# Kernel optimization log

Hardware: AMD Instinct MI355X
Metric: run time of the kernel (lower is better)

The kernel has to match this reference:

```python
import jax, jax.numpy as jnp
import numpy as np

TOP_K = 2
NORM_MIN = 1e-12
B, S, H = 2, 1024, 2048
E, I = 16, 1024
SHARED_I = 2048  # moe_intermediate_size * moe_num_shared_experts


def setup_inputs() -> dict:
    key = jax.random.key(0)
    ks = jax.random.split(key, 8)
    s = 0.02  # init scale
    return {
        "hidden_states": jax.random.normal(ks[0], (B, S, H), jnp.float32),
        "router_w": jax.random.normal(ks[1], (E, H), jnp.float32) * s,
        "w_gate": jax.random.normal(ks[2], (E, H, I), jnp.float32) * s,
        "w_up": jax.random.normal(ks[3], (E, H, I), jnp.float32) * s,
        "w_down": jax.random.normal(ks[4], (E, I, H), jnp.float32) * s,
        "ws_gate": jax.random.normal(ks[5], (H, SHARED_I), jnp.float32) * s,
        "ws_up": jax.random.normal(ks[6], (H, SHARED_I), jnp.float32) * s,
        "ws_down": jax.random.normal(ks[7], (SHARED_I, H), jnp.float32) * s,
    }


def reference(hidden_states, router_w, w_gate, w_up, w_down, ws_gate, ws_up, ws_down):
    b, s, h = hidden_states.shape
    x = hidden_states.reshape(-1, h)                      # [N, H]
    n = x.shape[0]

    # Router: float32 softmax -> top-k -> renormalize with clamp
    router_logits = x.astype(jnp.float32) @ router_w.T    # [N, E]
    probs = jax.nn.softmax(router_logits, axis=-1)
    rw, sel = jax.lax.top_k(probs, TOP_K)                 # [N, K]
    rw = rw / jnp.clip(rw.sum(axis=-1, keepdims=True), NORM_MIN)
    rw = rw.astype(x.dtype)

    # Dense combine weights [N, E] (equivalent to one_hot dispatch/scatter)
    combine = jnp.zeros((n, E), x.dtype).at[jnp.arange(n)[:, None], sel].set(rw)

    # All-expert SwiGLU MLP (full-capacity MoE, no dropped tokens)
    g = jnp.einsum('nh,ehi->eni', x, w_gate)              # [E, N, I]
    u = jnp.einsum('nh,ehi->eni', x, w_up)
    o = jnp.einsum('eni,eih->enh', jax.nn.silu(g) * u, w_down)  # [E, N, H]
    out = jnp.einsum('enh,ne->nh', o, combine)            # weighted combine

    # Shared expert path
    shared = (jax.nn.silu(x @ ws_gate) * (x @ ws_up)) @ ws_down
    out = out + shared

    return out.reshape(b, s, h), router_logits
```

## Files before the change

kernel.cpp:

```cpp
#include <hip/hip_runtime.h>
#include <cstdint>
#include <cstddef>
#include <cmath>

#define N_TOK 2048
#define HDIM  2048
#define NEXP  16
#define IDIM  1024
#define SIDIM 2048
#define NTHREADS 256

typedef __attribute__((ext_vector_type(8))) short bf16x8;
typedef __attribute__((ext_vector_type(4))) float f32x4;

__device__ __forceinline__ uint32_t f2bf_u(float f) {
    union { float f; uint32_t u; } v; v.f = f;
    return (v.u + 0x7FFFu + ((v.u >> 16) & 1u)) >> 16;
}
__device__ __forceinline__ uint32_t pack2bf(float lo, float hi) {
    return f2bf_u(lo) | (f2bf_u(hi) << 16);
}

__global__ __launch_bounds__(NTHREADS)
void router_kernel(const float* __restrict__ x,
                   const float* __restrict__ rw,
                   float* __restrict__ logits_out,
                   int* __restrict__ cnt,
                   int* __restrict__ tok_list,
                   float* __restrict__ wt_list)
{
    const int n = blockIdx.x;
    const int tid = threadIdx.x;
    const float* xr = x + (size_t)n * HDIM;

    float acc[NEXP];
#pragma unroll
    for (int e = 0; e < NEXP; ++e) acc[e] = 0.f;

    for (int h = tid; h < HDIM; h += NTHREADS) {
        float xv = xr[h];
#pragma unroll
        for (int e = 0; e < NEXP; ++e) acc[e] += xv * rw[(size_t)e * HDIM + h];
    }

    __shared__ float red[NEXP][NTHREADS];
#pragma unroll
    for (int e = 0; e < NEXP; ++e) red[e][tid] = acc[e];
    __syncthreads();
    for (int s = NTHREADS / 2; s > 0; s >>= 1) {
        if (tid < s) {
#pragma unroll
            for (int e = 0; e < NEXP; ++e) red[e][tid] += red[e][tid + s];
        }
        __syncthreads();
    }

    if (tid < NEXP) logits_out[(size_t)n * NEXP + tid] = red[tid][0];

    if (tid == 0) {
        float l[NEXP];
#pragma unroll
        for (int e = 0; e < NEXP; ++e) l[e] = red[e][0];
        int e0 = 0;
#pragma unroll
        for (int e = 1; e < NEXP; ++e) if (l[e] > l[e0]) e0 = e;
        int e1 = (e0 == 0) ? 1 : 0;
#pragma unroll
        for (int e = 0; e < NEXP; ++e)
            if (e != e0 && l[e] > l[e1]) e1 = e;
        float t = expf(l[e1] - l[e0]);
        float s = 1.f + t;
        float rw0 = 1.f / s;
        float rw1 = t / s;
        int p0 = atomicAdd(&cnt[e0], 1);
        tok_list[e0 * N_TOK + p0] = n;
        wt_list[e0 * N_TOK + p0] = rw0;
        int p1 = atomicAdd(&cnt[e1], 1);
        tok_list[e1 * N_TOK + p1] = n;
        wt_list[e1 * N_TOK + p1] = rw1;
    }
}

__global__ void prefix_kernel(const int* __restrict__ cnt, int* __restrict__ base)
{
    if (threadIdx.x == 0) {
        int s = 0;
        for (int e = 0; e < NEXP; ++e) { base[e] = s; s += cnt[e]; }
    }
}

__global__ __launch_bounds__(NTHREADS)
void dual_swiglu_mfma(const float* __restrict__ X,
                      const float* __restrict__ WgAll,
                      const float* __restrict__ WuAll,
                      unsigned short* __restrict__ Y,
                      const int* __restrict__ cnt,
                      const int* __restrict__ base,
                      const int* __restrict__ tok_list,
                      const int Icols)
{
    const int e  = blockIdx.z;
    const int m0 = blockIdx.y * 128;
    const int n0 = blockIdx.x * 64;
    const bool gathered = (tok_list != nullptr);
    const int M = gathered ? cnt[e] : N_TOK;
    if (m0 >= M) return;
    const float* Wg = WgAll + (size_t)e * HDIM * Icols;
    const float* Wu = WuAll + (size_t)e * HDIM * Icols;
    const int yb = gathered ? base[e] : 0;

    __shared__ short As[128][40];
    __shared__ short Gs[64][40];
    __shared__ short Us[64][40];

    const int tid  = threadIdx.x;
    const int lane = tid & 63;
    const int wave = tid >> 6;
    const int wm   = wave >> 1;
    const int wn   = wave & 1;
    const int l15  = lane & 15;
    const int q    = lane >> 4;

    const int ar = tid >> 1;
    const int ac = (tid & 1) * 16;
    const int slotA = m0 + ar;
    int xrow;
    if (gathered) xrow = tok_list[e * N_TOK + ((slotA < M) ? slotA : 0)];
    else          xrow = slotA;
    const float* xp = X + (size_t)xrow * HDIM + ac;

    const int wng = (tid & 15) << 2;
    const int wkp = (tid >> 4) << 1;
    const float* gp = Wg + (size_t)wkp * Icols + n0 + wng;
    const float* up = Wu + (size_t)wkp * Icols + n0 + wng;

    f32x4 accg[4][2], accu[4][2];
#pragma unroll
    for (int i = 0; i < 4; ++i)
#pragma unroll
        for (int j = 0; j < 2; ++j) {
            accg[i][j] = (f32x4){0.f, 0.f, 0.f, 0.f};
            accu[i][j] = (f32x4){0.f, 0.f, 0.f, 0.f};
        }

    for (int k0 = 0; k0 < HDIM; k0 += 32) {
        const float* xk = xp + k0;
        float4 xa = *(const float4*)(xk + 0);
        float4 xb = *(const float4*)(xk + 4);
        float4 xc = *(const float4*)(xk + 8);
        float4 xd = *(const float4*)(xk + 12);
        const float* gk = gp + (size_t)k0 * Icols;
        float4 g0 = *(const float4*)(gk);
        float4 g1 = *(const float4*)(gk + Icols);
        const float* uk = up + (size_t)k0 * Icols;
        float4 u0 = *(const float4*)(uk);
        float4 u1 = *(const float4*)(uk + Icols);

        __syncthreads();
        {
            uint4 w0 = make_uint4(pack2bf(xa.x, xa.y), pack2bf(xa.z, xa.w),
                                  pack2bf(xb.x, xb.y), pack2bf(xb.z, xb.w));
            uint4 w1 = make_uint4(pack2bf(xc.x, xc.y), pack2bf(xc.z, xc.w),
                                  pack2bf(xd.x, xd.y), pack2bf(xd.z, xd.w));
            *reinterpret_cast<uint4*>(&As[ar][ac])     = w0;
            *reinterpret_cast<uint4*>(&As[ar][ac + 8]) = w1;
        }
        ((uint32_t*)&Gs[wng + 0][wkp])[0] = pack2bf(g0.x, g1.x);
        ((uint32_t*)&Gs[wng + 1][wkp])[0] = pack2bf(g0.y, g1.y);
        ((uint32_t*)&Gs[wng + 2][wkp])[0] = pack2bf(g0.z, g1.z);
        ((uint32_t*)&Gs[wng + 3][wkp])[0] = pack2bf(g0.w, g1.w);
        ((uint32_t*)&Us[wng + 0][wkp])[0] = pack2bf(u0.x, u1.x);
        ((uint32_t*)&Us[wng + 1][wkp])[0] = pack2bf(u0.y, u1.y);
        ((uint32_t*)&Us[wng + 2][wkp])[0] = pack2bf(u0.z, u1.z);
        ((uint32_t*)&Us[wng + 3][wkp])[0] = pack2bf(u0.w, u1.w);
        __syncthreads();

        bf16x8 af[4], bg[2], bu[2];
#pragma unroll
        for (int i = 0; i < 4; ++i)
            af[i] = *reinterpret_cast<const bf16x8*>(&As[wm * 64 + i * 16 + l15][q * 8]);
#pragma unroll
        for (int j = 0; j < 2; ++j) {
            bg[j] = *reinterpret_cast<const bf16x8*>(&Gs[wn * 32 + j * 16 + l15][q * 8]);
            bu[j] = *reinterpret_cast<const bf16x8*>(&Us[wn * 32 + j * 16 + l15][q * 8]);
        }
#pragma unroll
        for (int i = 0; i < 4; ++i)
#pragma unroll
            for (int j = 0; j < 2; ++j) {
                accg[i][j] = __builtin_amdgcn_mfma_f32_16x16x32_bf16(af[i], bg[j], accg[i][j], 0, 0, 0);
                accu[i][j] = __builtin_amdgcn_mfma_f32_16x16x32_bf16(af[i], bu[j], accu[i][j], 0, 0, 0);
            }
    }

#pragma unroll
    for (int i = 0; i < 4; ++i) {
#pragma unroll
        for (int r = 0; r < 4; ++r) {
            const int slot = m0 + wm * 64 + i * 16 + q * 4 + r;
            if (slot < M) {
                unsigned short* yrow = Y + (size_t)(yb + slot) * Icols;
#pragma unroll
                for (int j = 0; j < 2; ++j) {
                    const int col = n0 + wn * 32 + j * 16 + l15;
                    float g = accg[i][j][r];
                    float u = accu[i][j][r];
                    float y = (g / (1.f + expf(-g))) * u;
                    yrow[col] = (unsigned short)f2bf_u(y);
                }
            }
        }
    }
}

__global__ __launch_bounds__(NTHREADS)
void down_mfma(const unsigned short* __restrict__ A,
               const float* __restrict__ WdAll,
               float* __restrict__ out,
               const int* __restrict__ cnt,
               const int* __restrict__ base,
               const int* __restrict__ tok_list,
               const float* __restrict__ wt_list,
               const int K)
{
    const int e  = blockIdx.z;
    const int m0 = blockIdx.y * 128;
    const int n0 = blockIdx.x * 128;
    const bool scatter = (tok_list != nullptr);
    const int M = scatter ? cnt[e] : N_TOK;
    if (m0 >= M) return;
    const float* Wd = WdAll + (size_t)e * K * HDIM;
    const int yb = scatter ? base[e] : 0;

    __shared__ short As[128][40];
    __shared__ short Bs[128][40];

    const int tid  = threadIdx.x;
    const int lane = tid & 63;
    const int wave = tid >> 6;
    const int wm   = wave >> 1;
    const int wn   = wave & 1;
    const int l15  = lane & 15;
    const int q    = lane >> 4;

    const int ar = tid >> 1;
    const int ac = (tid & 1) * 16;
    const int slotA = m0 + ar;
    const int arow = yb + ((slotA < M) ? slotA : 0);
    const unsigned short* ap = A + (size_t)arow * K + ac;

    const int bn = (tid & 31) << 2;
    const int bk = (tid >> 5) << 2;
    const float* bp = Wd + (size_t)bk * HDIM + n0 + bn;

    f32x4 acc[4][4];
#pragma unroll
    for (int i = 0; i < 4; ++i)
#pragma unroll
        for (int j = 0; j < 4; ++j) acc[i][j] = (f32x4){0.f, 0.f, 0.f, 0.f};

    for (int k0 = 0; k0 < K; k0 += 32) {
        uint4 a0 = *(const uint4*)(ap + k0);
        uint4 a1 = *(const uint4*)(ap + k0 + 8);
        const float* bkp = bp + (size_t)k0 * HDIM;
        float4 b0 = *(const float4*)(bkp);
        float4 b1 = *(const float4*)(bkp + HDIM);
        float4 b2 = *(const float4*)(bkp + 2 * (size_t)HDIM);
        float4 b3 = *(const float4*)(bkp + 3 * (size_t)HDIM);

        __syncthreads();
        *reinterpret_cast<uint4*>(&As[ar][ac])     = a0;
        *reinterpret_cast<uint4*>(&As[ar][ac + 8]) = a1;
        {
            uint2 w;
            w.x = pack2bf(b0.x, b1.x); w.y = pack2bf(b2.x, b3.x);
            *reinterpret_cast<uint2*>(&Bs[bn + 0][bk]) = w;
            w.x = pack2bf(b0.y, b1.y); w.y = pack2bf(b2.y, b3.y);
            *reinterpret_cast<uint2*>(&Bs[bn + 1][bk]) = w;
            w.x = pack2bf(b0.z, b1.z); w.y = pack2bf(b2.z, b3.z);
            *reinterpret_cast<uint2*>(&Bs[bn + 2][bk]) = w;
            w.x = pack2bf(b0.w, b1.w); w.y = pack2bf(b2.w, b3.w);
            *reinterpret_cast<uint2*>(&Bs[bn + 3][bk]) = w;
        }
        __syncthreads();

        bf16x8 af[4], bf[4];
#pragma unroll
        for (int i = 0; i < 4; ++i)
            af[i] = *reinterpret_cast<const bf16x8*>(&As[wm * 64 + i * 16 + l15][q * 8]);
#pragma unroll
        for (int j = 0; j < 4; ++j)
            bf[j] = *reinterpret_cast<const bf16x8*>(&Bs[wn * 64 + j * 16 + l15][q * 8]);
#pragma unroll
        for (int i = 0; i < 4; ++i)
#pragma unroll
            for (int j = 0; j < 4; ++j)
                acc[i][j] = __builtin_amdgcn_mfma_f32_16x16x32_bf16(af[i], bf[j], acc[i][j], 0, 0, 0);
    }

#pragma unroll
    for (int i = 0; i < 4; ++i) {
#pragma unroll
        for (int r = 0; r < 4; ++r) {
            const int slot = m0 + wm * 64 + i * 16 + q * 4 + r;
            if (slot >= M) continue;
            if (scatter) {
                const int tok = tok_list[e * N_TOK + slot];
                const float wt = wt_list[e * N_TOK + slot];
                float* orow = out + (size_t)tok * HDIM;
#pragma unroll
                for (int j = 0; j < 4; ++j) {
                    const int col = n0 + wn * 64 + j * 16 + l15;
                    atomicAdd(&orow[col], wt * acc[i][j][r]);
                }
            } else {
                float* orow = out + (size_t)slot * HDIM;
#pragma unroll
                for (int j = 0; j < 4; ++j) {
                    const int col = n0 + wn * 64 + j * 16 + l15;
                    orow[col] = acc[i][j][r];
                }
            }
        }
    }
}

extern "C" void kernel_launch(void* const* d_in, const int* in_sizes, int n_in,
                              void* d_out, int out_size, void* d_ws, size_t ws_size,
                              hipStream_t stream)
{
    const float* x       = (const float*)d_in[0];
    const float* rw      = (const float*)d_in[1];
    const float* w_gate  = (const float*)d_in[2];
    const float* w_up    = (const float*)d_in[3];
    const float* w_down  = (const float*)d_in[4];
    const float* ws_gate = (const float*)d_in[5];
    const float* ws_up   = (const float*)d_in[6];
    const float* ws_down = (const float*)d_in[7];

    float* out    = (float*)d_out;
    float* logits = out + (size_t)N_TOK * HDIM;

    char* w = (char*)d_ws;
    int* cnt      = (int*)w;
    int* base     = cnt + 16;
    int* tok_list = base + 16;
    float* wt_list = (float*)(tok_list + NEXP * N_TOK);
    uintptr_t p = (uintptr_t)(wt_list + NEXP * N_TOK);
    p = (p + 255) & ~(uintptr_t)255;
    unsigned short* A_shared = (unsigned short*)p;
    unsigned short* Ybuf     = A_shared + (size_t)N_TOK * SIDIM;

    hipMemsetAsync(cnt, 0, 16 * sizeof(int), stream);

    router_kernel<<<dim3(N_TOK), dim3(NTHREADS), 0, stream>>>(
        x, rw, logits, cnt, tok_list, wt_list);
    prefix_kernel<<<dim3(1), dim3(64), 0, stream>>>(cnt, base);

    dual_swiglu_mfma<<<dim3(SIDIM / 64, N_TOK / 128, 1), dim3(NTHREADS), 0, stream>>>(
        x, ws_gate, ws_up, A_shared, cnt, base, nullptr, SIDIM);
    down_mfma<<<dim3(HDIM / 128, N_TOK / 128, 1), dim3(NTHREADS), 0, stream>>>(
        A_shared, ws_down, out, cnt, base, nullptr, nullptr, SIDIM);

    dual_swiglu_mfma<<<dim3(IDIM / 64, N_TOK / 128, NEXP), dim3(NTHREADS), 0, stream>>>(
        x, w_gate, w_up, Ybuf, cnt, base, tok_list, IDIM);
    down_mfma<<<dim3(HDIM / 128, N_TOK / 128, NEXP), dim3(NTHREADS), 0, stream>>>(
        Ybuf, w_down, out, cnt, base, tok_list, wt_list, IDIM);
}
```

Before: 746.1 us.

## Pre-convert activations to bf16, prefetch next tile, swizzle LDS, shrink down-proj tile

New measurement: 713.3 us. 4.4% less time.

```diff
diff --git a/kernel.cpp b/kernel.cpp
--- a/kernel.cpp
+++ b/kernel.cpp
@@ -19,6 +19,21 @@
 }
 __device__ __forceinline__ uint32_t pack2bf(float lo, float hi) {
     return f2bf_u(lo) | (f2bf_u(hi) << 16);
+}
+
+__device__ __forceinline__ int swz(int row, int c) {
+    return row * 4 + (c ^ ((row >> 1) & 3));
+}
+
+__global__ __launch_bounds__(NTHREADS)
+void convert_x_kernel(const float* __restrict__ x, unsigned short* __restrict__ xb)
+{
+    const size_t i = ((size_t)blockIdx.x * NTHREADS + threadIdx.x) * 8;
+    float4 a = *(const float4*)(x + i);
+    float4 b = *(const float4*)(x + i + 4);
+    uint4 w = make_uint4(pack2bf(a.x, a.y), pack2bf(a.z, a.w),
+                         pack2bf(b.x, b.y), pack2bf(b.z, b.w));
+    *(uint4*)(xb + i) = w;
 }
 
 __global__ __launch_bounds__(NTHREADS)
@@ -90,7 +105,7 @@
 }
 
 __global__ __launch_bounds__(NTHREADS)
-void dual_swiglu_mfma(const float* __restrict__ X,
+void dual_swiglu_mfma(const unsigned short* __restrict__ Xb,
                       const float* __restrict__ WgAll,
                       const float* __restrict__ WuAll,
                       unsigned short* __restrict__ Y,
@@ -109,9 +124,9 @@
     const float* Wu = WuAll + (size_t)e * HDIM * Icols;
     const int yb = gathered ? base[e] : 0;
 
-    __shared__ short As[128][40];
-    __shared__ short Gs[64][40];
-    __shared__ short Us[64][40];
+    __shared__ short As[128 * 32];
+    __shared__ short Gs[64 * 32];
+    __shared__ short Us[64 * 32];
 
     const int tid  = threadIdx.x;
     const int lane = tid & 63;
@@ -122,17 +137,17 @@
     const int q    = lane >> 4;
 
     const int ar = tid >> 1;
-    const int ac = (tid & 1) * 16;
+    const int at = tid & 1;
     const int slotA = m0 + ar;
     int xrow;
-    if (gathered) xrow = tok_list[e * N_TOK + ((slotA < M) ? slotA : 0)];
+    if (gathered) xrow = tok_list[e * N_TOK + ((slotA < M) ? slotA : (M - 1))];
     else          xrow = slotA;
-    const float* xp = X + (size_t)xrow * HDIM + ac;
-
-    const int wng = (tid & 15) << 2;
-    const int wkp = (tid >> 4) << 1;
-    const float* gp = Wg + (size_t)wkp * Icols + n0 + wng;
-    const float* up = Wu + (size_t)wkp * Icols + n0 + wng;
+    const unsigned short* xp = Xb + (size_t)xrow * HDIM + at * 16;
+
+    const int wcn = tid & 63;
+    const int wcc = tid >> 6;
+    const float* gp = Wg + n0 + wcn;
+    const float* up = Wu + n0 + wcn;
 
     f32x4 accg[4][2], accu[4][2];
 #pragma unroll
@@ -143,46 +158,43 @@
             accu[i][j] = (f32x4){0.f, 0.f, 0.f, 0.f};
         }
 
+    uint4 a0, a1;
+    float g8[8], u8[8];
+    auto ldtile = [&](int kk) {
+        a0 = *(const uint4*)(xp + kk);
+        a1 = *(const uint4*)(xp + kk + 8);
+#pragma unroll
+        for (int j = 0; j < 8; ++j) {
+            g8[j] = gp[(size_t)(kk + wcc * 8 + j) * Icols];
+            u8[j] = up[(size_t)(kk + wcc * 8 + j) * Icols];
+        }
+    };
+
+    ldtile(0);
     for (int k0 = 0; k0 < HDIM; k0 += 32) {
-        const float* xk = xp + k0;
-        float4 xa = *(const float4*)(xk + 0);
-        float4 xb = *(const float4*)(xk + 4);
-        float4 xc = *(const float4*)(xk + 8);
-        float4 xd = *(const float4*)(xk + 12);
-        const float* gk = gp + (size_t)k0 * Icols;
-        float4 g0 = *(const float4*)(gk);
-        float4 g1 = *(const float4*)(gk + Icols);
-        const float* uk = up + (size_t)k0 * Icols;
-        float4 u0 = *(const float4*)(uk);
-        float4 u1 = *(const float4*)(uk + Icols);
-
-        __syncthreads();
-        {
-            uint4 w0 = make_uint4(pack2bf(xa.x, xa.y), pack2bf(xa.z, xa.w),
-                                  pack2bf(xb.x, xb.y), pack2bf(xb.z, xb.w));
-            uint4 w1 = make_uint4(pack2bf(xc.x, xc.y), pack2bf(xc.z, xc.w),
-                                  pack2bf(xd.x, xd.y), pack2bf(xd.z, xd.w));
-            *reinterpret_cast<uint4*>(&As[ar][ac])     = w0;
-            *reinterpret_cast<uint4*>(&As[ar][ac + 8]) = w1;
-        }
-        ((uint32_t*)&Gs[wng + 0][wkp])[0] = pack2bf(g0.x, g1.x);
-        ((uint32_t*)&Gs[wng + 1][wkp])[0] = pack2bf(g0.y, g1.y);
-        ((uint32_t*)&Gs[wng + 2][wkp])[0] = pack2bf(g0.z, g1.z);
-        ((uint32_t*)&Gs[wng + 3][wkp])[0] = pack2bf(g0.w, g1.w);
-        ((uint32_t*)&Us[wng + 0][wkp])[0] = pack2bf(u0.x, u1.x);
-        ((uint32_t*)&Us[wng + 1][wkp])[0] = pack2bf(u0.y, u1.y);
-        ((uint32_t*)&Us[wng + 2][wkp])[0] = pack2bf(u0.z, u1.z);
-        ((uint32_t*)&Us[wng + 3][wkp])[0] = pack2bf(u0.w, u1.w);
-        __syncthreads();
+        __syncthreads();
+        *(uint4*)(As + swz(ar, at * 2 + 0) * 8) = a0;
+        *(uint4*)(As + swz(ar, at * 2 + 1) * 8) = a1;
+        uint4 gw = make_uint4(pack2bf(g8[0], g8[1]), pack2bf(g8[2], g8[3]),
+                              pack2bf(g8[4], g8[5]), pack2bf(g8[6], g8[7]));
+        uint4 uw = make_uint4(pack2bf(u8[0], u8[1]), pack2bf(u8[2], u8[3]),
+                              pack2bf(u8[4], u8[5]), pack2bf(u8[6], u8[7]));
+        *(uint4*)(Gs + swz(wcn, wcc) * 8) = gw;
+        *(uint4*)(Us + swz(wcn, wcc) * 8) = uw;
+        __syncthreads();
+
+        int kn = k0 + 32;
+        if (kn >= HDIM) kn = k0;
+        ldtile(kn);
 
         bf16x8 af[4], bg[2], bu[2];
 #pragma unroll
         for (int i = 0; i < 4; ++i)
-            af[i] = *reinterpret_cast<const bf16x8*>(&As[wm * 64 + i * 16 + l15][q * 8]);
+            af[i] = *(const bf16x8*)(As + swz(wm * 64 + i * 16 + l15, q) * 8);
 #pragma unroll
         for (int j = 0; j < 2; ++j) {
-            bg[j] = *reinterpret_cast<const bf16x8*>(&Gs[wn * 32 + j * 16 + l15][q * 8]);
-            bu[j] = *reinterpret_cast<const bf16x8*>(&Us[wn * 32 + j * 16 + l15][q * 8]);
+            bg[j] = *(const bf16x8*)(Gs + swz(wn * 32 + j * 16 + l15, q) * 8);
+            bu[j] = *(const bf16x8*)(Us + swz(wn * 32 + j * 16 + l15, q) * 8);
         }
 #pragma unroll
         for (int i = 0; i < 4; ++i)
@@ -224,7 +236,7 @@
                const int K)
 {
     const int e  = blockIdx.z;
-    const int m0 = blockIdx.y * 128;
+    const int m0 = blockIdx.y * 64;
     const int n0 = blockIdx.x * 128;
     const bool scatter = (tok_list != nullptr);
     const int M = scatter ? cnt[e] : N_TOK;
@@ -232,8 +244,8 @@
     const float* Wd = WdAll + (size_t)e * K * HDIM;
     const int yb = scatter ? base[e] : 0;
 
-    __shared__ short As[128][40];
-    __shared__ short Bs[128][40];
+    __shared__ short As[64 * 32];
+    __shared__ short Bs[128 * 32];
 
     const int tid  = threadIdx.x;
     const int lane = tid & 63;
@@ -243,66 +255,68 @@
     const int l15  = lane & 15;
     const int q    = lane >> 4;
 
-    const int ar = tid >> 1;
-    const int ac = (tid & 1) * 16;
+    const int ar = tid >> 2;
+    const int ac = tid & 3;
     const int slotA = m0 + ar;
-    const int arow = yb + ((slotA < M) ? slotA : 0);
-    const unsigned short* ap = A + (size_t)arow * K + ac;
-
-    const int bn = (tid & 31) << 2;
-    const int bk = (tid >> 5) << 2;
-    const float* bp = Wd + (size_t)bk * HDIM + n0 + bn;
-
-    f32x4 acc[4][4];
-#pragma unroll
-    for (int i = 0; i < 4; ++i)
+    const int arow = yb + ((slotA < M) ? slotA : (M - 1));
+    const unsigned short* ap = A + (size_t)arow * K + ac * 8;
+
+    const int bn = tid & 127;
+    const int bh = tid >> 7;
+    const float* bp = Wd + n0 + bn;
+
+    f32x4 acc[2][4];
+#pragma unroll
+    for (int i = 0; i < 2; ++i)
 #pragma unroll
         for (int j = 0; j < 4; ++j) acc[i][j] = (f32x4){0.f, 0.f, 0.f, 0.f};
 
+    uint4 a0;
+    float b16[16];
+    auto ldtile = [&](int kk) {
+        a0 = *(const uint4*)(ap + kk);
+#pragma unroll
+        for (int c = 0; c < 2; ++c)
+#pragma unroll
+            for (int j = 0; j < 8; ++j)
+                b16[c * 8 + j] = bp[(size_t)(kk + (bh * 2 + c) * 8 + j) * HDIM];
+    };
+
+    ldtile(0);
     for (int k0 = 0; k0 < K; k0 += 32) {
-        uint4 a0 = *(const uint4*)(ap + k0);
-        uint4 a1 = *(const uint4*)(ap + k0 + 8);
-        const float* bkp = bp + (size_t)k0 * HDIM;
-        float4 b0 = *(const float4*)(bkp);
-        float4 b1 = *(const float4*)(bkp + HDIM);
-        float4 b2 = *(const float4*)(bkp + 2 * (size_t)HDIM);
-        float4 b3 = *(const float4*)(bkp + 3 * (size_t)HDIM);
-
-        __syncthreads();
-        *reinterpret_cast<uint4*>(&As[ar][ac])     = a0;
-        *reinterpret_cast<uint4*>(&As[ar][ac + 8]) = a1;
-        {
-            uint2 w;
-            w.x = pack2bf(b0.x, b1.x); w.y = pack2bf(b2.x, b3.x);
-            *reinterpret_cast<uint2*>(&Bs[bn + 0][bk]) = w;
-            w.x = pack2bf(b0.y, b1.y); w.y = pack2bf(b2.y, b3.y);
-            *reinterpret_cast<uint2*>(&Bs[bn + 1][bk]) = w;
-            w.x = pack2bf(b0.z, b1.z); w.y = pack2bf(b2.z, b3.z);
-            *reinterpret_cast<uint2*>(&Bs[bn + 2][bk]) = w;
-            w.x = pack2bf(b0.w, b1.w); w.y = pack2bf(b2.w, b3.w);
-            *reinterpret_cast<uint2*>(&Bs[bn + 3][bk]) = w;
-        }
-        __syncthreads();
-
-        bf16x8 af[4], bf[4];
-#pragma unroll
-        for (int i = 0; i < 4; ++i)
-            af[i] = *reinterpret_cast<const bf16x8*>(&As[wm * 64 + i * 16 + l15][q * 8]);
+        __syncthreads();
+        *(uint4*)(As + swz(ar, ac) * 8) = a0;
+        uint4 w0 = make_uint4(pack2bf(b16[0], b16[1]), pack2bf(b16[2], b16[3]),
+                              pack2bf(b16[4], b16[5]), pack2bf(b16[6], b16[7]));
+        uint4 w1 = make_uint4(pack2bf(b16[8], b16[9]), pack2bf(b16[10], b16[11]),
+                              pack2bf(b16[12], b16[13]), pack2bf(b16[14], b16[15]));
+        *(uint4*)(Bs + swz(bn, bh * 2 + 0) * 8) = w0;
+        *(uint4*)(Bs + swz(bn, bh * 2 + 1) * 8) = w1;
+        __syncthreads();
+
+        int kn = k0 + 32;
+        if (kn >= K) kn = k0;
+        ldtile(kn);
+
+        bf16x8 af[2], bfr[4];
+#pragma unroll
+        for (int i = 0; i < 2; ++i)
+            af[i] = *(const bf16x8*)(As + swz(wm * 32 + i * 16 + l15, q) * 8);
 #pragma unroll
         for (int j = 0; j < 4; ++j)
-            bf[j] = *reinterpret_cast<const bf16x8*>(&Bs[wn * 64 + j * 16 + l15][q * 8]);
-#pragma unroll
-        for (int i = 0; i < 4; ++i)
+            bfr[j] = *(const bf16x8*)(Bs + swz(wn * 64 + j * 16 + l15, q) * 8);
+#pragma unroll
+        for (int i = 0; i < 2; ++i)
 #pragma unroll
             for (int j = 0; j < 4; ++j)
-                acc[i][j] = __builtin_amdgcn_mfma_f32_16x16x32_bf16(af[i], bf[j], acc[i][j], 0, 0, 0);
-    }
-
-#pragma unroll
-    for (int i = 0; i < 4; ++i) {
+                acc[i][j] = __builtin_amdgcn_mfma_f32_16x16x32_bf16(af[i], bfr[j], acc[i][j], 0, 0, 0);
+    }
+
+#pragma unroll
+    for (int i = 0; i < 2; ++i) {
 #pragma unroll
         for (int r = 0; r < 4; ++r) {
-            const int slot = m0 + wm * 64 + i * 16 + q * 4 + r;
+            const int slot = m0 + wm * 32 + i * 16 + q * 4 + r;
             if (slot >= M) continue;
             if (scatter) {
                 const int tok = tok_list[e * N_TOK + slot];
@@ -348,22 +362,24 @@
     float* wt_list = (float*)(tok_list + NEXP * N_TOK);
     uintptr_t p = (uintptr_t)(wt_list + NEXP * N_TOK);
     p = (p + 255) & ~(uintptr_t)255;
-    unsigned short* A_shared = (unsigned short*)p;
+    unsigned short* Xb       = (unsigned short*)p;
+    unsigned short* A_shared = Xb + (size_t)N_TOK * HDIM;
     unsigned short* Ybuf     = A_shared + (size_t)N_TOK * SIDIM;
 
     hipMemsetAsync(cnt, 0, 16 * sizeof(int), stream);
 
+    convert_x_kernel<<<dim3((N_TOK * HDIM) / (NTHREADS * 8)), dim3(NTHREADS), 0, stream>>>(x, Xb);
     router_kernel<<<dim3(N_TOK), dim3(NTHREADS), 0, stream>>>(
         x, rw, logits, cnt, tok_list, wt_list);
     prefix_kernel<<<dim3(1), dim3(64), 0, stream>>>(cnt, base);
 
     dual_swiglu_mfma<<<dim3(SIDIM / 64, N_TOK / 128, 1), dim3(NTHREADS), 0, stream>>>(
-        x, ws_gate, ws_up, A_shared, cnt, base, nullptr, SIDIM);
-    down_mfma<<<dim3(HDIM / 128, N_TOK / 128, 1), dim3(NTHREADS), 0, stream>>>(
+        Xb, ws_gate, ws_up, A_shared, cnt, base, nullptr, SIDIM);
+    down_mfma<<<dim3(HDIM / 128, N_TOK / 64, 1), dim3(NTHREADS), 0, stream>>>(
         A_shared, ws_down, out, cnt, base, nullptr, nullptr, SIDIM);
 
     dual_swiglu_mfma<<<dim3(IDIM / 64, N_TOK / 128, NEXP), dim3(NTHREADS), 0, stream>>>(
-        x, w_gate, w_up, Ybuf, cnt, base, tok_list, IDIM);
-    down_mfma<<<dim3(HDIM / 128, N_TOK / 128, NEXP), dim3(NTHREADS), 0, stream>>>(
+        Xb, w_gate, w_up, Ybuf, cnt, base, tok_list, IDIM);
+    down_mfma<<<dim3(HDIM / 128, N_TOK / 64, NEXP), dim3(NTHREADS), 0, stream>>>(
         Ybuf, w_down, out, cnt, base, tok_list, wt_list, IDIM);
 }
```
